# Kernel optimization log

Measured on AMD Instinct MI355X. Metric: run time of the kernel, lower is better.

## Reference

```python
import jax, jax.numpy as jnp
import numpy as np

D_MODEL = 1024
QK_DIM = 1024
V_DIM = 1024
H = 16
TAU = 20.0
HQK = QK_DIM // H
HV = V_DIM // H
SCALE = HQK ** -0.5
SCALE_BASE = 512.0
EPS_GAMMA = 1e-8
EPS_GN = 1e-5


def _rotate_every_two(x):
    x1 = x[..., ::2]
    x2 = x[..., 1::2]
    return jnp.stack([-x2, x1], axis=-1).reshape(x.shape)


def _xpos_rotate(q, k, t):
    # q,k: (B,H,N,d); t: (B,N) continuous positions (timestamps in days)
    d = q.shape[-1]
    inv_freq = (1.0 / (10000.0 ** (np.arange(0, d, 2) / d))).astype(np.float32)  # (d/2,)
    sinusoid = t[:, None, :, None] * inv_freq  # (B,1,N,d/2)
    sin = jnp.repeat(jnp.sin(sinusoid), 2, axis=-1)  # (B,1,N,d)
    cos = jnp.repeat(jnp.cos(sinusoid), 2, axis=-1)
    scale_vec = ((np.arange(0, d, 2) + 0.4 * d) / (1.4 * d)).astype(np.float32)  # (d/2,)
    scale = jnp.repeat(scale_vec ** (t[:, None, :, None] / SCALE_BASE), 2, axis=-1)  # (B,1,N,d)
    q_rot = (q * cos + _rotate_every_two(q) * sin) * scale
    k_rot = (k * cos + _rotate_every_two(k) * sin) / scale
    return q_rot, k_rot


def setup_inputs() -> dict:
    key = jax.random.key(0)
    ks = jax.random.split(key, 6)
    B, N = 4, 1024
    X = jax.random.normal(ks[0], (B, N, D_MODEL), dtype=jnp.float32)
    # increasing timestamps in days
    timestamps = jnp.sort(jax.random.uniform(ks[1], (B, N), jnp.float32, 0.0, 100.0), axis=-1)
    W_qkv = jax.random.normal(ks[2], (D_MODEL, 2 * QK_DIM + V_DIM), dtype=jnp.float32) * 0.02
    W_gamma = jax.random.normal(ks[3], (D_MODEL, H), dtype=jnp.float32) * 0.02
    W_gated = jax.random.normal(ks[4], (D_MODEL, V_DIM), dtype=jnp.float32) * 0.02
    W_out = jax.random.normal(ks[5], (V_DIM, D_MODEL), dtype=jnp.float32) * 0.02
    return {"X": X, "timestamps": timestamps, "W_qkv": W_qkv, "W_gamma": W_gamma,
            "W_gated": W_gated, "W_out": W_out}


def reference(X, timestamps, W_qkv, W_gamma, W_gated, W_out):
    B, N, _ = X.shape
    qkv = X @ W_qkv  # (B,N,2*qk+v)
    q, k, v = jnp.split(qkv, [QK_DIM, 2 * QK_DIM], axis=-1)
    q = q.reshape(B, N, H, HQK).transpose(0, 2, 1, 3)  # (B,H,N,dk)
    k = k.reshape(B, N, H, HQK).transpose(0, 2, 1, 3)
    v = v.reshape(B, N, H, HV).transpose(0, 2, 1, 3)
    q, k = _xpos_rotate(q, k, timestamps)
    # data-dependent decay gamma in (0,1]
    gamma = jax.nn.sigmoid(X @ W_gamma) ** (1.0 / TAU)  # (B,N,H)
    log_b = jnp.cumsum(jnp.log(gamma + EPS_GAMMA), axis=1).transpose(0, 2, 1)  # (B,H,N)
    log_D = log_b[..., :, None] - log_b[..., None, :]  # (B,H,N,N)
    causal = jnp.tril(jnp.ones((N, N), dtype=bool))
    # masked_fill(-inf) then clamp[-80,0]: clip maps -inf -> -80 (matches torch)
    D = jnp.exp(jnp.clip(jnp.where(causal, log_D, -jnp.inf), -80.0, 0.0))
    attn = jnp.einsum('bhnd,bhmd->bhnm', q, k) * SCALE * D
    O = jnp.einsum('bhnm,bhmd->bhnd', attn, v)  # (B,H,N,dv)
    O = O.transpose(0, 2, 1, 3).reshape(B, N, V_DIM)
    # GroupNorm(num_groups=H, affine=False) over (channels-in-group, seq)
    g = O.reshape(B, N, H, HV)
    mu = g.mean(axis=(1, 3), keepdims=True)
    var = g.var(axis=(1, 3), keepdims=True)
    O = ((g - mu) / jnp.sqrt(var + EPS_GN)).reshape(B, N, V_DIM)
    O = jax.nn.silu(X @ W_gated) * O
    return O @ W_out
```

## Files before the change

kernel.cpp:

```cpp
#include <hip/hip_runtime.h>
#include <cstddef>
#include <cstdint>

#define NH 16
#define HD 64
#define NSEQ 1024
#define NB 4
#define DM 1024
#define SCALE 0.125f

typedef __attribute__((ext_vector_type(8))) short v8s;
typedef __attribute__((ext_vector_type(4))) float v4f;

__device__ __forceinline__ short f2bf(float x) {
    union { float f; unsigned u; } v; v.f = x;
    unsigned r = v.u + 0x7FFF + ((v.u >> 16) & 1);
    return (short)(r >> 16);
}
__device__ __forceinline__ float bf2f(short x) {
    union { unsigned u; float f; } v; v.u = ((unsigned)(unsigned short)x) << 16;
    return v.f;
}
__device__ __forceinline__ void gload16(const void* g, void* l) {
    __builtin_amdgcn_global_load_lds(
        (const __attribute__((address_space(1))) void*)g,
        (__attribute__((address_space(3))) void*)l, 16, 0, 0);
}
__device__ __forceinline__ int gswz(int r, int kbyte) {
    return (r * 64 + kbyte) ^ (((r >> 1) & 3) << 4);
}
__device__ __forceinline__ int aswz(int r, int byte) {
    return (r * 128 + byte) ^ ((r & 7) << 4);
}
#define SBAR() __builtin_amdgcn_s_barrier()
#define WAITV0() asm volatile("s_waitcnt vmcnt(0)" ::: "memory")
#define WAITV4() asm volatile("s_waitcnt vmcnt(4)" ::: "memory")
#define WAITL() asm volatile("s_waitcnt lgkmcnt(0)" ::: "memory")

__global__ __launch_bounds__(256) void prep_inputs(const float* __restrict__ X,
                                                   const float* __restrict__ ts,
                                                   const float* __restrict__ Wq,
                                                   const float* __restrict__ Wg,
                                                   const float* __restrict__ Wgt,
                                                   const float* __restrict__ Wo,
                                                   short* __restrict__ Wtq,
                                                   short* __restrict__ Wtg,
                                                   short* __restrict__ Wto,
                                                   float* __restrict__ loggam,
                                                   short* __restrict__ Xb,
                                                   float4* __restrict__ tbl) {
    __shared__ float smem[1024 * 17];
    const int bid = blockIdx.x;
    const int tid = threadIdx.x;
    if (bid < 1280) {
        short (*lsm)[136] = (short(*)[136])smem;
        int ct = bid % 40;
        const int kt = bid / 40;
        const float* W; short* Bt; int N;
        if (ct < 24)      { W = Wq;  Bt = Wtq; N = 3072; }
        else if (ct < 32) { W = Wgt; Bt = Wtg; N = 1024; ct -= 24; }
        else              { W = Wo;  Bt = Wto; N = 1024; ct -= 32; }
        {
            const int kk = tid >> 3, nn0 = (tid & 7) * 16;
            const float* src = W + (size_t)(kt * 32 + kk) * N + ct * 128 + nn0;
#pragma unroll
            for (int j = 0; j < 16; j += 4) {
                float4 v = *(const float4*)(src + j);
                lsm[kk][nn0 + j] = f2bf(v.x); lsm[kk][nn0 + j + 1] = f2bf(v.y);
                lsm[kk][nn0 + j + 2] = f2bf(v.z); lsm[kk][nn0 + j + 3] = f2bf(v.w);
            }
        }
        __syncthreads();
        const int rloc = tid >> 1, kb0 = (tid & 1) * 16;
        short o[16] __attribute__((aligned(16)));
#pragma unroll
        for (int j = 0; j < 16; ++j) o[j] = lsm[kb0 + j][rloc];
        char* base = (char*)(Bt + ((size_t)ct * 32 + kt) * 4096);
#pragma unroll
        for (int c = 0; c < 2; ++c)
            *(v8s*)(base + gswz(rloc, kb0 * 2 + c * 16)) = *(v8s*)&o[c * 8];
    } else if (bid < 1536) {
        float* wgs = smem;
#pragma unroll
        for (int it = 0; it < 16; ++it) {
            const int idx = it * 1024 + tid * 4;
            float4 v = *(const float4*)(Wg + idx);
            const int k = idx >> 4, h0 = idx & 15;
            wgs[k * 17 + h0]     = v.x;
            wgs[k * 17 + h0 + 1] = v.y;
            wgs[k * 17 + h0 + 2] = v.z;
            wgs[k * 17 + h0 + 3] = v.w;
        }
        __syncthreads();
        const int r = tid >> 4, c = tid & 15;
        const int row = (bid - 1280) * 16 + r;
        const int rt = row >> 7, rloc = row & 127;
        char* xtile = (char*)(Xb + (size_t)rt * 32 * 4096);
        const float* xrow = X + (size_t)row * DM;
        float acc[16];
#pragma unroll
        for (int h = 0; h < 16; ++h) acc[h] = 0.0f;
#pragma unroll 4
        for (int i = 0; i < 16; ++i) {
            const int kb = i * 64 + c * 4;
            float4 xv = *(const float4*)(xrow + kb);
            short4 o4 = make_short4(f2bf(xv.x), f2bf(xv.y), f2bf(xv.z), f2bf(xv.w));
            *(short4*)(xtile + (size_t)(kb >> 5) * 8192 + gswz(rloc, (kb & 31) * 2)) = o4;
            const float xs[4] = {xv.x, xv.y, xv.z, xv.w};
#pragma unroll
            for (int j = 0; j < 4; ++j) {
                const float* wrow = &wgs[(kb + j) * 17];
#pragma unroll
                for (int h = 0; h < 16; ++h) acc[h] = fmaf(xs[j], wrow[h], acc[h]);
            }
        }
#pragma unroll
        for (int h = 0; h < 16; ++h) {
#pragma unroll
            for (int off = 8; off >= 1; off >>= 1)
                acc[h] += __shfl_xor(acc[h], off, 16);
        }
        const float d = acc[c];
        const float sig = 1.0f / (1.0f + expf(-d));
        const float gam = powf(sig, 1.0f / 20.0f);
        loggam[(size_t)row * NH + c] = logf(gam + 1e-8f);
    } else {
        const int e = (bid - 1536) * 256 + tid;
        const int row = e >> 5, f = e & 31;
        const float tv = ts[row];
        const float inv_freq = exp2f(-0.4152410119f * (float)f);
        const float ang = tv * inv_freq;
        const float s = sinf(ang), c = cosf(ang);
        const float sv = ((float)(2 * f) + 25.6f) * (1.0f / 89.6f);
        const float ee = log2f(sv) * tv * (1.0f / 512.0f);
        tbl[e] = make_float4(c, s, exp2f(ee) * SCALE, exp2f(-ee));
    }
}

template<int MODE>
__global__ __launch_bounds__(256) void gemm_tt(const short* __restrict__ A,
                                               const short* __restrict__ B,
                                               void* __restrict__ C, int N,
                                               const short* __restrict__ O,
                                               const float* __restrict__ partial) {
    __shared__ short As[4096];
    __shared__ short Bs[4096];
    const int tid = threadIdx.x;
    const int w = tid >> 6, l = tid & 63;
    const int wr = w >> 1, wc = w & 1;
    const int rt = blockIdx.y, ct = blockIdx.x;
    const char* Abase = (const char*)A + ((size_t)rt * 32) * 8192;
    const char* Bbase = (const char*)B + ((size_t)ct * 32) * 8192;

    v4f acc[4][4];
#pragma unroll
    for (int i = 0; i < 4; ++i)
#pragma unroll
        for (int j = 0; j < 4; ++j) acc[i][j] = (v4f){0.f, 0.f, 0.f, 0.f};

    for (int kt = 0; kt < 32; ++kt) {
        __syncthreads();
#pragma unroll
        for (int i = 0; i < 2; ++i) {
            const int c = w * 2 + i;
            gload16(Abase + (size_t)kt * 8192 + c * 1024 + l * 16, (char*)As + c * 1024);
            gload16(Bbase + (size_t)kt * 8192 + c * 1024 + l * 16, (char*)Bs + c * 1024);
        }
        __syncthreads();
        v8s af[4], bfr[4];
#pragma unroll
        for (int i = 0; i < 4; ++i) {
            const int ra = wr * 64 + i * 16 + (l & 15);
            af[i] = *(const v8s*)((char*)As + gswz(ra, (l >> 4) * 16));
            const int rb = wc * 64 + i * 16 + (l & 15);
            bfr[i] = *(const v8s*)((char*)Bs + gswz(rb, (l >> 4) * 16));
        }
#pragma unroll
        for (int i = 0; i < 4; ++i)
#pragma unroll
            for (int j = 0; j < 4; ++j)
                acc[i][j] = __builtin_amdgcn_mfma_f32_16x16x32_bf16(af[i], bfr[j], acc[i][j], 0, 0, 0);
    }
    float mu = 0.f, rstd = 0.f;
    if (MODE == 2) {
        const int hh = ct * 2 + wc;
        const int bh = (rt >> 3) * NH + hh;
        float s = 0.f, q = 0.f;
#pragma unroll
        for (int i = 0; i < 8; ++i) {
            s += partial[(bh * 8 + i) * 2];
            q += partial[(bh * 8 + i) * 2 + 1];
        }
        const float inv = 1.0f / (NSEQ * HD);
        mu = s * inv;
        rstd = rsqrtf(q * inv - mu * mu + 1e-5f);
    }
#pragma unroll
    for (int i = 0; i < 4; ++i)
#pragma unroll
        for (int j = 0; j < 4; ++j) {
            const int r0 = rt * 128 + wr * 64 + i * 16 + (l >> 4) * 4;
            const int cc = ct * 128 + wc * 64 + j * 16 + (l & 15);
#pragma unroll
            for (int t2 = 0; t2 < 4; ++t2) {
                if (MODE == 1) ((short*)C)[(size_t)(r0 + t2) * N + cc] = f2bf(acc[i][j][t2]);
                else if (MODE == 0) ((float*)C)[(size_t)(r0 + t2) * N + cc] = acc[i][j][t2];
                else {
                    const int row = r0 + t2;
                    const float g = acc[i][j][t2];
                    const float silu = g / (1.0f + __expf(-g));
                    const float ov = bf2f(O[(size_t)row * DM + cc]);
                    const float val = silu * (ov - mu) * rstd;
                    const int rloc = row - rt * 128;
                    char* base = (char*)((short*)C + ((size_t)rt * 32 + (cc >> 5)) * 4096);
                    *(short*)(base + gswz(rloc, (cc & 31) * 2)) = f2bf(val);
                }
            }
        }
}

__global__ __launch_bounds__(256) void scan_kernel(const float* __restrict__ lg,
                                                   float* __restrict__ lgT) {
    const int wave = threadIdx.x >> 6;
    const int lane = threadIdx.x & 63;
    const int bh = blockIdx.x * 4 + wave;
    const int b = bh >> 4, h = bh & 15;
    const float* p = lg + (size_t)b * NSEQ * NH + h;
    const int n0 = lane * 16;
    float v[16];
    float s = 0.0f;
#pragma unroll
    for (int j = 0; j < 16; ++j) { v[j] = p[(size_t)(n0 + j) * NH]; s += v[j]; }
    float sc = s;
#pragma unroll
    for (int off = 1; off < 64; off <<= 1) {
        float o = __shfl_up(sc, off, 64);
        if (lane >= off) sc += o;
    }
    float acc = sc - s;
    float* q = lgT + (size_t)bh * NSEQ + n0;
#pragma unroll
    for (int j = 0; j < 16; ++j) { acc += v[j]; q[j] = acc; }
}

__global__ __launch_bounds__(256) void prep(const short* __restrict__ qkvb,
                                            const float4* __restrict__ tbl,
                                            short* __restrict__ Qb,
                                            short* __restrict__ Kb,
                                            short* __restrict__ Vtb) {
    __shared__ short vsm[64][72];
    const int tile = blockIdx.x, bh = blockIdx.y;
    const int b = bh >> 4, h = bh & 15;
    const int t = threadIdx.x;
    const int rloc = t >> 2, d0 = (t & 3) * 16;
    const int row = b * NSEQ + tile * 64 + rloc;
    const short* src = qkvb + (size_t)row * 3072 + h * HD;
    const size_t tb = ((size_t)bh * 16 + tile) * 4096;

    float qa[16], ka[16];
    {
        v8s q0 = *(const v8s*)(src + d0), q1 = *(const v8s*)(src + d0 + 8);
        v8s k0 = *(const v8s*)(src + 1024 + d0), k1 = *(const v8s*)(src + 1024 + d0 + 8);
#pragma unroll
        for (int j = 0; j < 8; ++j) {
            qa[j] = bf2f(q0[j]); qa[j + 8] = bf2f(q1[j]);
            ka[j] = bf2f(k0[j]); ka[j + 8] = bf2f(k1[j]);
        }
    }
    short qo[16] __attribute__((aligned(16)));
    short ko[16] __attribute__((aligned(16)));
#pragma unroll
    for (int j = 0; j < 8; ++j) {
        const int i = (d0 >> 1) + j;
        const float4 T = tbl[row * 32 + i];
        const float c = T.x, s = T.y, sc = T.z, isc = T.w;
        qo[2 * j]     = f2bf((qa[2 * j] * c - qa[2 * j + 1] * s) * sc);
        qo[2 * j + 1] = f2bf((qa[2 * j + 1] * c + qa[2 * j] * s) * sc);
        ko[2 * j]     = f2bf((ka[2 * j] * c - ka[2 * j + 1] * s) * isc);
        ko[2 * j + 1] = f2bf((ka[2 * j + 1] * c + ka[2 * j] * s) * isc);
    }
#pragma unroll
    for (int c = 0; c < 2; ++c) {
        *(v8s*)((char*)(Qb + tb) + aswz(rloc, d0 * 2 + c * 16)) = *(v8s*)&qo[c * 8];
        *(v8s*)((char*)(Kb + tb) + aswz(rloc, d0 * 2 + c * 16)) = *(v8s*)&ko[c * 8];
    }
    {
        v8s v0 = *(const v8s*)(src + 2048 + d0), v1 = *(const v8s*)(src + 2048 + d0 + 8);
        *(short4*)&vsm[rloc][d0]      = *(short4*)&v0;
        *(short4*)&vsm[rloc][d0 + 4]  = *((short4*)&v0 + 1);
        *(short4*)&vsm[rloc][d0 + 8]  = *(short4*)&v1;
        *(short4*)&vsm[rloc][d0 + 12] = *((short4*)&v1 + 1);
    }
    __syncthreads();
    {
        const int d = t >> 2, m0 = (t & 3) * 16;
        short vt[16] __attribute__((aligned(16)));
#pragma unroll
        for (int j = 0; j < 16; ++j) vt[j] = vsm[m0 + j][d];
#pragma unroll
        for (int c = 0; c < 2; ++c)
            *(v8s*)((char*)(Vtb + tb) + aswz(d, m0 * 2 + c * 16)) = *(v8s*)&vt[c * 8];
    }
}

__global__ __launch_bounds__(256) void attn6(const short* __restrict__ Qb,
                                             const short* __restrict__ Kb,
                                             const short* __restrict__ Vtb,
                                             const float* __restrict__ logbT,
                                             short* __restrict__ O,
                                             float* __restrict__ partial) {
    __shared__ short Ks[2][4096];
    __shared__ short Vts[2][4096];
    __shared__ short Ps[8192];
    __shared__ float lbAll[1024];
    __shared__ float emAll[1024];
    const int id = blockIdx.x;
    const int half = id >> 8;
    const int idx = id & 255;
    const int bh = ((idx & 7) << 3) | ((idx >> 3) & 7);
    const int qq = half == 0 ? (4 + (idx >> 6)) : (3 - (idx >> 6));
    const int b = bh >> 4, h = bh & 15;
    const int tid = threadIdx.x;
    const int w = tid >> 6, l = tid & 63;
    const int n0 = qq * 128;
    const int NT = 2 * qq + 2;

#pragma unroll
    for (int i = 0; i < 4; ++i) {
        const int c = w * 4 + i;
        gload16((const char*)Qb + ((size_t)bh * 16 + 2 * qq) * 8192 + c * 1024 + l * 16,
                (char*)Ps + c * 1024);
    }
    for (int i = tid; i < 1024; i += 256)
        lbAll[i] = logbT[(size_t)bh * NSEQ + i];
    WAITV0(); WAITL();
    SBAR();

    const float base = lbAll[n0];
    for (int i = tid; i < NT * 64; i += 256) emAll[i] = __expf(base - lbAll[i]);
    float en[2];
#pragma unroll
    for (int rg = 0; rg < 2; ++rg)
        en[rg] = __expf(lbAll[n0 + w * 32 + rg * 16 + (l & 15)] - base);
    v8s aq[2][2];
#pragma unroll
    for (int rg = 0; rg < 2; ++rg)
#pragma unroll
        for (int kc = 0; kc < 2; ++kc) {
            const int r = w * 32 + rg * 16 + (l & 15);
            aq[rg][kc] = *(const v8s*)((char*)Ps + (r >> 6) * 8192 +
                                       aswz(r & 63, kc * 64 + (l >> 4) * 16));
        }
    WAITL();
    SBAR();

    v4f oacc[2][4];
#pragma unroll
    for (int rg = 0; rg < 2; ++rg)
#pragma unroll
        for (int dt = 0; dt < 4; ++dt) oacc[rg][dt] = (v4f){0.f, 0.f, 0.f, 0.f};

#pragma unroll
    for (int i = 0; i < 2; ++i) {
        const int c = w * 2 + i;
        gload16((const char*)Kb + ((size_t)bh * 16 + 0) * 8192 + c * 1024 + l * 16,
                (char*)Ks + c * 1024);
        gload16((const char*)Vtb + ((size_t)bh * 16 + 0) * 8192 + c * 1024 + l * 16,
                (char*)Vts + c * 1024);
    }

    for (int t = 0; t < NT; ++t) {
        const int m0 = t * 64;
        const int buf = t & 1;
        SBAR();
        if (t + 1 < NT) {
            const int nb = (t + 1) & 1;
#pragma unroll
            for (int i = 0; i < 2; ++i) {
                const int c = w * 2 + i;
                gload16((const char*)Kb + ((size_t)bh * 16 + t + 1) * 8192 + c * 1024 + l * 16,
                        (char*)Ks + nb * 8192 + c * 1024);
                gload16((const char*)Vtb + ((size_t)bh * 16 + t + 1) * 8192 + c * 1024 + l * 16,
                        (char*)Vts + nb * 8192 + c * 1024);
            }
            WAITV4();
        } else {
            WAITV0();
        }
        SBAR();

        const bool active = (m0 <= n0 + w * 32 + 31);
        if (active) {
            const char* KsB = (const char*)Ks + buf * 8192;
            const char* VtsB = (const char*)Vts + buf * 8192;
            v4f sfr[2][4];
#pragma unroll
            for (int rg = 0; rg < 2; ++rg)
#pragma unroll
                for (int m4 = 0; m4 < 4; ++m4) sfr[rg][m4] = (v4f){0.f, 0.f, 0.f, 0.f};
            __builtin_amdgcn_s_setprio(1);
#pragma unroll
            for (int m4 = 0; m4 < 4; ++m4) {
#pragma unroll
                for (int kc = 0; kc < 2; ++kc) {
                    const int m = m4 * 16 + (l & 15);
                    v8s bk = *(const v8s*)(KsB + aswz(m, kc * 64 + (l >> 4) * 16));
#pragma unroll
                    for (int rg = 0; rg < 2; ++rg)
                        sfr[rg][m4] = __builtin_amdgcn_mfma_f32_16x16x32_bf16(bk, aq[rg][kc], sfr[rg][m4], 0, 0, 0);
                }
            }
            __builtin_amdgcn_s_setprio(0);
            const bool needMask = (m0 + 63) > (n0 + w * 32);
#pragma unroll
            for (int rg = 0; rg < 2; ++rg) {
                const int r = w * 32 + rg * 16 + (l & 15);
                const float enr = en[rg];
#pragma unroll
                for (int m4 = 0; m4 < 4; ++m4) {
                    const int mbase = m0 + m4 * 16 + (l >> 4) * 4;
                    float4 emv = *(const float4*)&emAll[mbase];
                    const float ems[4] = {emv.x, emv.y, emv.z, emv.w};
                    union { short s[4]; uint2 u; } pk;
#pragma unroll
                    for (int t2 = 0; t2 < 4; ++t2) {
                        float sval = sfr[rg][m4][t2] * enr * ems[t2];
                        if (needMask && (n0 + r) < (mbase + t2)) sval = 0.0f;
                        pk.s[t2] = f2bf(sval);
                    }
                    *(uint2*)((char*)Ps + aswz(r, (m4 * 16 + (l >> 4) * 4) * 2)) = pk.u;
                }
            }
            WAITL();
            __builtin_amdgcn_sched_barrier(0);
            __builtin_amdgcn_s_setprio(1);
#pragma unroll
            for (int kc = 0; kc < 2; ++kc) {
                v8s ap[2];
#pragma unroll
                for (int rg = 0; rg < 2; ++rg) {
                    const int r = w * 32 + rg * 16 + (l & 15);
                    ap[rg] = *(const v8s*)((char*)Ps + aswz(r, kc * 64 + (l >> 4) * 16));
                }
#pragma unroll
                for (int dt = 0; dt < 4; ++dt) {
                    const int d = dt * 16 + (l & 15);
                    v8s bv = *(const v8s*)(VtsB + aswz(d, kc * 64 + (l >> 4) * 16));
#pragma unroll
                    for (int rg = 0; rg < 2; ++rg)
                        oacc[rg][dt] = __builtin_amdgcn_mfma_f32_16x16x32_bf16(bv, ap[rg], oacc[rg][dt], 0, 0, 0);
                }
            }
            __builtin_amdgcn_s_setprio(0);
        }
    }
    float psum = 0.0f, pssq = 0.0f;
#pragma unroll
    for (int rg = 0; rg < 2; ++rg) {
        const int row = n0 + w * 32 + rg * 16 + (l & 15);
#pragma unroll
        for (int dt = 0; dt < 4; ++dt) {
            const float a0 = oacc[rg][dt][0], a1 = oacc[rg][dt][1];
            const float a2 = oacc[rg][dt][2], a3 = oacc[rg][dt][3];
            short4 o4 = make_short4(f2bf(a0), f2bf(a1), f2bf(a2), f2bf(a3));
            *(short4*)(O + (size_t)(b * NSEQ + row) * DM + h * HD + dt * 16 + (l >> 4) * 4) = o4;
            psum += a0 + a1 + a2 + a3;
            pssq += a0 * a0 + a1 * a1 + a2 * a2 + a3 * a3;
        }
    }
    __syncthreads();
    float* red = (float*)Ks;
    red[tid] = psum; red[256 + tid] = pssq;
    __syncthreads();
    for (int s = 128; s > 0; s >>= 1) {
        if (tid < s) { red[tid] += red[tid + s]; red[256 + tid] += red[256 + tid + s]; }
        __syncthreads();
    }
    if (tid == 0) {
        partial[(bh * 8 + qq) * 2]     = red[0];
        partial[(bh * 8 + qq) * 2 + 1] = red[256];
    }
}

extern "C" void kernel_launch(void* const* d_in, const int* in_sizes, int n_in,
                              void* d_out, int out_size, void* d_ws, size_t ws_size,
                              hipStream_t stream) {
    const float* X       = (const float*)d_in[0];
    const float* ts      = (const float*)d_in[1];
    const float* W_qkv   = (const float*)d_in[2];
    const float* W_gamma = (const float*)d_in[3];
    const float* W_gated = (const float*)d_in[4];
    const float* W_out   = (const float*)d_in[5];
    float* out = (float*)d_out;

    char* ws = (char*)d_ws;
    short*  Xb    = (short*)(ws + 0);
    short*  Wtq   = (short*)(ws + 8388608);
    short*  Wtg   = (short*)(ws + 14680064);
    short*  Wto   = (short*)(ws + 16777216);
    short*  Qb    = (short*)(ws + 18874368);
    short*  Kb    = (short*)(ws + 27262976);
    short*  Vtb   = (short*)(ws + 35651584);
    float*  logb  = (float*)(ws + 44040192);
    float*  logbT = (float*)(ws + 44302336);
    float4* tbl   = (float4*)(ws + 44564480);
    short*  Oatt  = (short*)(ws + 46661632);
    float*  partial = (float*)(ws + 55050240);
    short*  Gb    = (short*)(ws + 55054336);
    short*  qkvb  = (short*)(ws + 63442944);

    prep_inputs<<<2048, 256, 0, stream>>>(X, ts, W_qkv, W_gamma, W_gated, W_out,
                                          Wtq, Wtg, Wto, logb, Xb, tbl);
    scan_kernel<<<16, 256, 0, stream>>>(logb, logbT);
    gemm_tt<1><<<dim3(24, 32), 256, 0, stream>>>(Xb, Wtq, qkvb, 3072, nullptr, nullptr);
    prep<<<dim3(16, 64), 256, 0, stream>>>(qkvb, tbl, Qb, Kb, Vtb);
    attn6<<<512, 256, 0, stream>>>(Qb, Kb, Vtb, logbT, Oatt, partial);
    gemm_tt<2><<<dim3(8, 32), 256, 0, stream>>>(Xb, Wtg, Gb, 1024, Oatt, partial);
    gemm_tt<0><<<dim3(8, 32), 256, 0, stream>>>(Gb, Wto, out, 1024, nullptr, nullptr);
}
```

Before: 153.2 us.

## Write V transposed from GEMM epilogue and triple-buffer K/V in attention

Splits the QKV projection so the V part is computed by a separate GEMM launch whose epilogue stores V directly in the transposed, swizzled tile layout. This removes the LDS transpose and the extra V round trip from the prep kernel. The attention kernel now uses a three-stage K/V buffer ring with two tiles prefetched, so only one barrier per iteration is needed. The costs are an extra kernel launch, smaller GEMM grids, more LDS per block (which may reduce occupancy), and scattered 8-byte epilogue stores.

```diff
diff --git a/kernel.cpp b/kernel.cpp
--- a/kernel.cpp
+++ b/kernel.cpp
@@ -201,11 +201,24 @@
         for (int j = 0; j < 4; ++j) {
             const int r0 = rt * 128 + wr * 64 + i * 16 + (l >> 4) * 4;
             const int cc = ct * 128 + wc * 64 + j * 16 + (l & 15);
+            if (MODE == 3) {
+                const int h = ct * 2 + wc;
+                const int d = j * 16 + (l & 15);
+                const int b = r0 >> 10;
+                const int tile = (r0 >> 6) & 15;
+                const int m0 = r0 & 63;
+                union { short s[4]; uint2 u; } pk;
+#pragma unroll
+                for (int t2 = 0; t2 < 4; ++t2) pk.s[t2] = f2bf(acc[i][j][t2]);
+                char* base = (char*)C + ((size_t)((b * 16 + h) * 16 + tile)) * 8192;
+                *(uint2*)(base + aswz(d, m0 * 2)) = pk.u;
+                continue;
+            }
 #pragma unroll
             for (int t2 = 0; t2 < 4; ++t2) {
                 if (MODE == 1) ((short*)C)[(size_t)(r0 + t2) * N + cc] = f2bf(acc[i][j][t2]);
                 else if (MODE == 0) ((float*)C)[(size_t)(r0 + t2) * N + cc] = acc[i][j][t2];
-                else {
+                else if (MODE == 2) {
                     const int row = r0 + t2;
                     const float g = acc[i][j][t2];
                     const float silu = g / (1.0f + __expf(-g));
@@ -246,15 +259,13 @@
 __global__ __launch_bounds__(256) void prep(const short* __restrict__ qkvb,
                                             const float4* __restrict__ tbl,
                                             short* __restrict__ Qb,
-                                            short* __restrict__ Kb,
-                                            short* __restrict__ Vtb) {
-    __shared__ short vsm[64][72];
+                                            short* __restrict__ Kb) {
     const int tile = blockIdx.x, bh = blockIdx.y;
     const int b = bh >> 4, h = bh & 15;
     const int t = threadIdx.x;
     const int rloc = t >> 2, d0 = (t & 3) * 16;
     const int row = b * NSEQ + tile * 64 + rloc;
-    const short* src = qkvb + (size_t)row * 3072 + h * HD;
+    const short* src = qkvb + (size_t)row * 2048 + h * HD;
     const size_t tb = ((size_t)bh * 16 + tile) * 4096;
 
     float qa[16], ka[16];
@@ -284,33 +295,15 @@
         *(v8s*)((char*)(Qb + tb) + aswz(rloc, d0 * 2 + c * 16)) = *(v8s*)&qo[c * 8];
         *(v8s*)((char*)(Kb + tb) + aswz(rloc, d0 * 2 + c * 16)) = *(v8s*)&ko[c * 8];
     }
-    {
-        v8s v0 = *(const v8s*)(src + 2048 + d0), v1 = *(const v8s*)(src + 2048 + d0 + 8);
-        *(short4*)&vsm[rloc][d0]      = *(short4*)&v0;
-        *(short4*)&vsm[rloc][d0 + 4]  = *((short4*)&v0 + 1);
-        *(short4*)&vsm[rloc][d0 + 8]  = *(short4*)&v1;
-        *(short4*)&vsm[rloc][d0 + 12] = *((short4*)&v1 + 1);
-    }
-    __syncthreads();
-    {
-        const int d = t >> 2, m0 = (t & 3) * 16;
-        short vt[16] __attribute__((aligned(16)));
-#pragma unroll
-        for (int j = 0; j < 16; ++j) vt[j] = vsm[m0 + j][d];
-#pragma unroll
-        for (int c = 0; c < 2; ++c)
-            *(v8s*)((char*)(Vtb + tb) + aswz(d, m0 * 2 + c * 16)) = *(v8s*)&vt[c * 8];
-    }
-}
-
-__global__ __launch_bounds__(256) void attn6(const short* __restrict__ Qb,
+}
+
+__global__ __launch_bounds__(256) void attn7(const short* __restrict__ Qb,
                                              const short* __restrict__ Kb,
                                              const short* __restrict__ Vtb,
                                              const float* __restrict__ logbT,
                                              short* __restrict__ O,
                                              float* __restrict__ partial) {
-    __shared__ short Ks[2][4096];
-    __shared__ short Vts[2][4096];
+    __shared__ short KV[3][2][4096];
     __shared__ short Ps[8192];
     __shared__ float lbAll[1024];
     __shared__ float emAll[1024];
@@ -361,38 +354,38 @@
         for (int dt = 0; dt < 4; ++dt) oacc[rg][dt] = (v4f){0.f, 0.f, 0.f, 0.f};
 
 #pragma unroll
-    for (int i = 0; i < 2; ++i) {
-        const int c = w * 2 + i;
-        gload16((const char*)Kb + ((size_t)bh * 16 + 0) * 8192 + c * 1024 + l * 16,
-                (char*)Ks + c * 1024);
-        gload16((const char*)Vtb + ((size_t)bh * 16 + 0) * 8192 + c * 1024 + l * 16,
-                (char*)Vts + c * 1024);
+    for (int tt = 0; tt < 2; ++tt) {
+#pragma unroll
+        for (int i = 0; i < 2; ++i) {
+            const int c = w * 2 + i;
+            gload16((const char*)Kb + ((size_t)bh * 16 + tt) * 8192 + c * 1024 + l * 16,
+                    (char*)KV[tt][0] + c * 1024);
+            gload16((const char*)Vtb + ((size_t)bh * 16 + tt) * 8192 + c * 1024 + l * 16,
+                    (char*)KV[tt][1] + c * 1024);
+        }
     }
 
     for (int t = 0; t < NT; ++t) {
         const int m0 = t * 64;
-        const int buf = t & 1;
+        const int buf = t % 3;
+        if (t + 1 < NT) { WAITV4(); } else { WAITV0(); }
         SBAR();
-        if (t + 1 < NT) {
-            const int nb = (t + 1) & 1;
+        if (t + 2 < NT) {
+            const int nb = (t + 2) % 3;
 #pragma unroll
             for (int i = 0; i < 2; ++i) {
                 const int c = w * 2 + i;
-                gload16((const char*)Kb + ((size_t)bh * 16 + t + 1) * 8192 + c * 1024 + l * 16,
-                        (char*)Ks + nb * 8192 + c * 1024);
-                gload16((const char*)Vtb + ((size_t)bh * 16 + t + 1) * 8192 + c * 1024 + l * 16,
-                        (char*)Vts + nb * 8192 + c * 1024);
-            }
-            WAITV4();
-        } else {
-            WAITV0();
-        }
-        SBAR();
+                gload16((const char*)Kb + ((size_t)bh * 16 + t + 2) * 8192 + c * 1024 + l * 16,
+                        (char*)KV[nb][0] + c * 1024);
+                gload16((const char*)Vtb + ((size_t)bh * 16 + t + 2) * 8192 + c * 1024 + l * 16,
+                        (char*)KV[nb][1] + c * 1024);
+            }
+        }
 
         const bool active = (m0 <= n0 + w * 32 + 31);
         if (active) {
-            const char* KsB = (const char*)Ks + buf * 8192;
-            const char* VtsB = (const char*)Vts + buf * 8192;
+            const char* KsB = (const char*)KV[buf][0];
+            const char* VtsB = (const char*)KV[buf][1];
             v4f sfr[2][4];
 #pragma unroll
             for (int rg = 0; rg < 2; ++rg)
@@ -469,7 +462,7 @@
         }
     }
     __syncthreads();
-    float* red = (float*)Ks;
+    float* red = (float*)KV;
     red[tid] = psum; red[256 + tid] = pssq;
     __syncthreads();
     for (int s = 128; s > 0; s >>= 1) {
@@ -512,9 +505,11 @@
     prep_inputs<<<2048, 256, 0, stream>>>(X, ts, W_qkv, W_gamma, W_gated, W_out,
                                           Wtq, Wtg, Wto, logb, Xb, tbl);
     scan_kernel<<<16, 256, 0, stream>>>(logb, logbT);
-    gemm_tt<1><<<dim3(24, 32), 256, 0, stream>>>(Xb, Wtq, qkvb, 3072, nullptr, nullptr);
-    prep<<<dim3(16, 64), 256, 0, stream>>>(qkvb, tbl, Qb, Kb, Vtb);
-    attn6<<<512, 256, 0, stream>>>(Qb, Kb, Vtb, logbT, Oatt, partial);
+    gemm_tt<1><<<dim3(16, 32), 256, 0, stream>>>(Xb, Wtq, qkvb, 2048, nullptr, nullptr);
+    gemm_tt<3><<<dim3(8, 32), 256, 0, stream>>>(Xb, Wtq + (size_t)16 * 32 * 4096, Vtb, 1024,
+                                                nullptr, nullptr);
+    prep<<<dim3(16, 64), 256, 0, stream>>>(qkvb, tbl, Qb, Kb);
+    attn7<<<512, 256, 0, stream>>>(Qb, Kb, Vtb, logbT, Oatt, partial);
     gemm_tt<2><<<dim3(8, 32), 256, 0, stream>>>(Xb, Wtg, Gb, 1024, Oatt, partial);
     gemm_tt<0><<<dim3(8, 32), 256, 0, stream>>>(Gb, Wto, out, 1024, nullptr, nullptr);
 }
```

New measurement: 171.7 us. 12.0% more time.
